# Performance work log

Measured on AMD Instinct MI355X. Metric: run time of the kernel, lower is better.

## Reference

```python
import jax, jax.numpy as jnp
import numpy as np

B, S, E = 2, 2048, 1024
HID = 1024
HEADS = 16
EPS = 1e-5
SCALE = (E * 2) ** (-0.5)  # source uses input_data_dim*2


def setup_inputs() -> dict:
    key = jax.random.key(0)
    k1, k2, k3 = jax.random.split(key, 3)
    return {
        "x": jax.random.normal(k1, (B, S, E), dtype=jnp.float32),
        "ln_g": jnp.ones((E,), jnp.float32),
        "ln_b": jnp.zeros((E,), jnp.float32),
        "W1": jax.random.normal(k2, (E, 3 * HID), jnp.float32) * 0.02,
        "b1": jnp.zeros((3 * HID,), jnp.float32),
        "W2": jax.random.normal(k3, (HID, HID), jnp.float32) * 0.02,
        "b2": jnp.zeros((HID,), jnp.float32),
    }


def reference(x, ln_g, ln_b, W1, b1, W2, b2):
    # LayerNorm over last dim
    mu = jnp.mean(x, axis=-1, keepdims=True)
    var = jnp.mean(jnp.square(x - mu), axis=-1, keepdims=True)
    xn = (x - mu) * jax.lax.rsqrt(var + EPS) * ln_g + ln_b
    # QKV projection: [B,S,3*HID]
    qkv = jnp.einsum('bse,ef->bsf', xn, W1) + b1
    # Faithful to source: flat reshape to (heads, B, S, 3*HID/heads)
    qkv_heads = qkv.reshape(HEADS, B, S, -1)
    q, k, v = jnp.split(qkv_heads, 3, axis=-1)  # each [H,B,S,d]
    scores = jnp.einsum('hbse,hbSe->hbsS', q, k) * SCALE  # [H,B,S,S]
    att = jax.nn.softmax(scores, axis=-1)
    full_att = jnp.einsum('hbsS,hbSe->hbse', att, v)  # [H,B,S,d]
    full_att = full_att.reshape(B, S, -1)  # faithful flat reshape -> [B,S,HID]
    out = jnp.einsum('bsh,hk->bsk', full_att, W2) + b2
    return out
```

## Files before the change

kernel.cpp:

```cpp
#include <hip/hip_runtime.h>

typedef unsigned short u16;
typedef __bf16 bf16x8 __attribute__((ext_vector_type(8)));
typedef float f32x4 __attribute__((ext_vector_type(4)));

static constexpr float SCALE2 = 0.022097086912079608f * 1.4426950408889634f;

__device__ __forceinline__ u16 f2b(float f) {
  union { float f; unsigned int i; } v; v.f = f;
  unsigned int r = v.i + 0x7fffu + ((v.i >> 16) & 1u);
  return (u16)(r >> 16);
}
__device__ __forceinline__ unsigned int pk2(float a, float b) {
#if __has_builtin(__builtin_amdgcn_cvt_pk_bf16_f32)
  auto v = __builtin_amdgcn_cvt_pk_bf16_f32(a, b);
  unsigned int u;
  __builtin_memcpy(&u, &v, 4);
  return u;
#else
  union { float f; unsigned int i; } x, y; x.f = a; y.f = b;
  return ((x.i + 0x8000u) >> 16) | ((y.i + 0x8000u) & 0xffff0000u);
#endif
}
__device__ __forceinline__ void async16(const u16* g, u16* l) {
  __builtin_amdgcn_global_load_lds((const __attribute__((address_space(1))) void*)g,
                                   (__attribute__((address_space(3))) void*)l,
                                   16, 0, 0);
}

__global__ __launch_bounds__(256) void ln_kernel(const float* __restrict__ x,
                                                 const float* __restrict__ g,
                                                 const float* __restrict__ b,
                                                 u16* __restrict__ xn) {
  const int row = blockIdx.x;
  const int t = threadIdx.x;
  float4 v = *(const float4*)(x + (size_t)row * 1024 + t * 4);
  float s = v.x + v.y + v.z + v.w;
  float ss = v.x * v.x + v.y * v.y + v.z * v.z + v.w * v.w;
  for (int off = 32; off >= 1; off >>= 1) {
    s += __shfl_xor(s, off, 64);
    ss += __shfl_xor(ss, off, 64);
  }
  __shared__ float red[8];
  const int w = t >> 6;
  if ((t & 63) == 0) { red[w] = s; red[4 + w] = ss; }
  __syncthreads();
  s = red[0] + red[1] + red[2] + red[3];
  ss = red[4] + red[5] + red[6] + red[7];
  const float mu = s * (1.0f / 1024.0f);
  const float var = ss * (1.0f / 1024.0f) - mu * mu;
  const float inv = rsqrtf(var + 1e-5f);
  float4 gg = *(const float4*)(g + t * 4);
  float4 bb = *(const float4*)(b + t * 4);
  ushort4 o;
  o.x = f2b((v.x - mu) * inv * gg.x + bb.x);
  o.y = f2b((v.y - mu) * inv * gg.y + bb.y);
  o.z = f2b((v.z - mu) * inv * gg.z + bb.z);
  o.w = f2b((v.w - mu) * inv * gg.w + bb.w);
  *(ushort4*)(xn + (size_t)row * 1024 + t * 4) = o;
}

__global__ __launch_bounds__(256) void transpose2_k(const float* __restrict__ W1,
                                                    u16* __restrict__ W1T,
                                                    const float* __restrict__ W2,
                                                    u16* __restrict__ W2T) {
  const int z = blockIdx.z;
  if (z == 1 && blockIdx.x >= 16) return;
  const int C = z ? 1024 : 3072;
  const float* in = z ? W2 : W1;
  u16* out = z ? W2T : W1T;
  __shared__ u16 tile[64 * 72];
  const int c0 = blockIdx.x * 64, r0 = blockIdx.y * 64;
  const int t = threadIdx.x;
  const int row = t >> 2, cseg = t & 3;
  for (int it = 0; it < 4; it++) {
    float4 v = *(const float4*)&in[(size_t)(r0 + row) * C + c0 + it * 16 + cseg * 4];
    ushort4 o;
    o.x = f2b(v.x); o.y = f2b(v.y); o.z = f2b(v.z); o.w = f2b(v.w);
    *(ushort4*)&tile[row * 72 + it * 16 + cseg * 4] = o;
  }
  __syncthreads();
  const int orow = t >> 2, ch = t & 3;
  u16 vals[16];
  for (int j = 0; j < 16; j++) vals[j] = tile[(ch * 16 + j) * 72 + orow];
  u16* dp = out + (size_t)(c0 + orow) * 1024 + r0 + ch * 16;
  *(uint4*)&dp[0] = *(uint4*)&vals[0];
  *(uint4*)&dp[8] = *(uint4*)&vals[8];
}

template <int MODE, int MT>
__global__ __launch_bounds__(256) void gemm_bt(const u16* __restrict__ A,
                                               const u16* __restrict__ Bt,
                                               const float* __restrict__ bias,
                                               float* __restrict__ C,
                                               int M, int N, int K,
                                               u16* __restrict__ Qc,
                                               u16* __restrict__ Kc,
                                               u16* __restrict__ Vtmp) {
  __shared__ __align__(16) u16 SMEM[8192];
  u16* As = SMEM;
  u16* Bs = SMEM + MT * 32;
  const int m0 = blockIdx.y * MT, n0 = blockIdx.x * 128;
  const int t = threadIdx.x, w = t >> 6, lane = t & 63;
  const int q = lane >> 4, l16 = lane & 15;
  const int wm = (w >> 1) * (MT / 2), wn = (w & 1) * 64;
  constexpr int NI = MT / 32;

  const int sc = (lane & 3) ^ ((lane >> 3) & 3);
  const u16* ap = A + (size_t)(m0 + w * 16 + (lane >> 2)) * K + sc * 8;
  const u16* bp = Bt + (size_t)(n0 + w * 16 + (lane >> 2)) * K + sc * 8;
  u16* lA = &As[w * 512];
  u16* lB = &Bs[w * 512];
  const int ac = q ^ ((l16 >> 1) & 3);

  f32x4 acc[NI][4];
  const f32x4 zero = {0.f, 0.f, 0.f, 0.f};
  for (int i = 0; i < NI; i++)
    for (int j = 0; j < 4; j++) acc[i][j] = zero;

  for (int k0 = 0; k0 < K; k0 += 32) {
    for (int i = 0; i < MT / 64; i++)
      async16(ap + (size_t)(i * 64) * K, lA + i * 2048);
    for (int i = 0; i < 2; i++)
      async16(bp + (size_t)(i * 64) * K, lB + i * 2048);
    ap += 32; bp += 32;
    __syncthreads();
    bf16x8 af[NI], bfr[4];
    for (int i = 0; i < NI; i++)
      af[i] = *(const bf16x8*)&As[(wm + i * 16 + l16) * 32 + ac * 8];
    for (int j = 0; j < 4; j++)
      bfr[j] = *(const bf16x8*)&Bs[(wn + j * 16 + l16) * 32 + ac * 8];
    for (int i = 0; i < NI; i++)
      for (int j = 0; j < 4; j++)
        acc[i][j] = __builtin_amdgcn_mfma_f32_16x16x32_bf16(af[i], bfr[j], acc[i][j], 0, 0, 0);
    __syncthreads();
  }

  if constexpr (MODE == 0) {
    for (int j = 0; j < 4; j++) {
      const int col = n0 + wn + j * 16 + l16;
      const float bv = bias[col];
      for (int i = 0; i < NI; i++) {
        const int rbase = m0 + wm + i * 16 + q * 4;
        for (int r = 0; r < 4; r++)
          C[(size_t)(rbase + r) * N + col] = acc[i][j][r] + bv;
      }
    }
  } else {
    const int seg = n0 + wn;
    const int k64 = seg >> 6;
    const int tcol = k64 / 3;
    const int typ = k64 - tcol * 3;
    u16* dst = (typ == 0) ? Qc : (typ == 1) ? Kc : Vtmp;
    const int gidx = m0 >> 7;
    u16* tw = &SMEM[w * 1280];
    float bv[4];
    for (int j = 0; j < 4; j++) bv[j] = bias[seg + j * 16 + l16];
    __syncthreads();
    for (int i = 0; i < 4; i++) {
      for (int j = 0; j < 4; j++) {
        ushort4 pk;
        pk.x = f2b(acc[i][j][0] + bv[j]);
        pk.y = f2b(acc[i][j][1] + bv[j]);
        pk.z = f2b(acc[i][j][2] + bv[j]);
        pk.w = f2b(acc[i][j][3] + bv[j]);
        *(ushort4*)&tw[(j * 16 + l16) * 20 + q * 4] = pk;
      }
      const int r2 = lane >> 2;
      const int quarter = lane & 3;
      u16 vals[16];
      for (int c = 0; c < 16; c++)
        vals[c] = tw[(quarter * 16 + c) * 20 + r2];
      const int lr = wm + i * 16 + r2;
      const int s = (lr << 4) + tcol;
      u16* dp = dst + ((size_t)gidx * 2048 + s) * 64 + quarter * 16;
      *(uint4*)&dp[0] = *(uint4*)&vals[0];
      *(uint4*)&dp[8] = *(uint4*)&vals[8];
    }
  }
}

__global__ __launch_bounds__(256) void vtrans(const u16* __restrict__ Vtmp,
                                              u16* __restrict__ Vt) {
  __shared__ __align__(16) u16 tile[64 * 64];
  const int g = blockIdx.y, s0 = blockIdx.x * 64;
  const int t = threadIdx.x;
  const int row = t >> 3, ch = t & 7;
  for (int p = 0; p < 2; p++) {
    const int r = p * 32 + row;
    uint4 v = *(const uint4*)&Vtmp[((size_t)g * 2048 + s0 + r) * 64 + ch * 8];
    *(uint4*)&tile[r * 64 + ((ch ^ (r & 7)) * 8)] = v;
  }
  __syncthreads();
  const int d = t >> 2, scn = t & 3;
  u16 vals[16];
  for (int j2 = 0; j2 < 16; j2++) {
    const int s = scn * 16 + j2;
    vals[j2] = tile[s * 64 + (((d >> 3) ^ (s & 7)) * 8) + (d & 7)];
  }
  u16* dp = Vt + ((size_t)g * 64 + d) * 2048 + s0 + scn * 16;
  *(uint4*)&dp[0] = *(uint4*)&vals[0];
  *(uint4*)&dp[8] = *(uint4*)&vals[8];
}

__global__ __launch_bounds__(256) void attn_kernel(const u16* __restrict__ Qc,
                                                   const u16* __restrict__ Kc,
                                                   const u16* __restrict__ Vt,
                                                   u16* __restrict__ Oc) {
  __shared__ __align__(16) u16 LDS[32768];
  u16* Ks = LDS;
  u16* Vs = LDS + 8192;
  u16* Ps = LDS + 16384;
  const int g = blockIdx.y;
  const int q0 = blockIdx.x * 128;
  const int t = threadIdx.x, w = t >> 6, lane = t & 63;
  const int q = lane >> 4, l16 = lane & 15;

  const u16* Qg = Qc + (size_t)g * 2048 * 64;
  const u16* Kg = Kc + (size_t)g * 2048 * 64;
  const u16* Vg = Vt + (size_t)g * 64 * 2048;

  bf16x8 aq[2][2];
  for (int rt = 0; rt < 2; rt++)
    for (int ks = 0; ks < 2; ks++)
      aq[rt][ks] = *(const bf16x8*)&Qg[(size_t)(q0 + w * 32 + rt * 16 + l16) * 64 + ks * 32 + q * 8];

  f32x4 accO[2][4];
  const f32x4 zero = {0.f, 0.f, 0.f, 0.f};
  for (int rt = 0; rt < 2; rt++)
    for (int c = 0; c < 4; c++) accO[rt][c] = zero;
  f32x4 psv[2] = {zero, zero};

  const int kc = (lane & 7) ^ ((lane >> 3) & 7);
  const int vc = (lane & 15) ^ ((w * 4 + (lane >> 4)) & 7);
  const u16* kp = Kg + (size_t)(w * 8 + (lane >> 3)) * 64 + kc * 8;
  const u16* vp = Vg + (size_t)(w * 4 + (lane >> 4)) * 2048 + vc * 8;
  u16* lK = &Ks[w * 512];
  u16* lV = &Vs[w * 512];

  const int kch = q ^ (l16 & 7);
  const int pbase = w * 4096;
  const int pxor = l16 & 3;

  for (int it = 0; it < 16; it++) {
    const int kt0 = it * 128;
    for (int i = 0; i < 4; i++) {
      async16(kp + (size_t)kt0 * 64 + i * 2048, lK + i * 2048);
      async16(vp + kt0 + (size_t)i * 32768, lV + i * 2048);
    }
    __syncthreads();

    f32x4 sa[2][8];
    for (int ct = 0; ct < 8; ct++) {
      bf16x8 bk0 = *(const bf16x8*)&Ks[(ct * 16 + l16) * 64 + kch * 8];
      bf16x8 bk1 = *(const bf16x8*)&Ks[(ct * 16 + l16) * 64 + (kch ^ 4) * 8];
      for (int rt = 0; rt < 2; rt++) {
        f32x4 a = zero;
        a = __builtin_amdgcn_mfma_f32_16x16x32_bf16(bk0, aq[rt][0], a, 0, 0, 0);
        a = __builtin_amdgcn_mfma_f32_16x16x32_bf16(bk1, aq[rt][1], a, 0, 0, 0);
        sa[rt][ct] = a;
      }
    }

    for (int rt = 0; rt < 2; rt++) {
      const int sbase = pbase + rt * 2048 + l16 * 32;
      for (int ct = 0; ct < 8; ct++) {
        f32x4 p;
        for (int r = 0; r < 4; r++) p[r] = __builtin_amdgcn_exp2f(sa[rt][ct][r] * SCALE2);
        psv[rt] += p;
        uint2 pk;
        pk.x = pk2(p[0], p[1]);
        pk.y = pk2(p[2], p[3]);
        const int c2 = ((ct & 1) * 2 + (q >> 1)) ^ pxor;
        *(uint2*)&Ps[sbase + (ct >> 1) * 512 + c2 * 8 + (q & 1) * 4] = pk;
      }
    }

    for (int ks2 = 0; ks2 < 4; ks2++) {
      bf16x8 apf[2];
      for (int rt = 0; rt < 2; rt++)
        apf[rt] = *(const bf16x8*)&Ps[pbase + rt * 2048 + ks2 * 512 + l16 * 32 + (q ^ pxor) * 8];
      for (int c = 0; c < 4; c++) {
        const int vch = (ks2 * 4 + q) ^ (l16 & 7);
        bf16x8 bv = *(const bf16x8*)&Vs[(c * 16 + l16) * 128 + vch * 8];
        for (int rt = 0; rt < 2; rt++)
          accO[rt][c] = __builtin_amdgcn_mfma_f32_16x16x32_bf16(bv, apf[rt], accO[rt][c], 0, 0, 0);
      }
    }
    __syncthreads();
  }

  for (int rt = 0; rt < 2; rt++) {
    float lsum = psv[rt][0] + psv[rt][1] + psv[rt][2] + psv[rt][3];
    lsum += __shfl_xor(lsum, 16, 64);
    lsum += __shfl_xor(lsum, 32, 64);
    const int srow = q0 + w * 32 + rt * 16 + l16;
    const int orow = g * 128 + (srow >> 4);
    const int cbase = (srow & 15) * 64;
    const float linv = 1.0f / lsum;
    for (int c = 0; c < 4; c++) {
      ushort4 o;
      o.x = f2b(accO[rt][c][0] * linv);
      o.y = f2b(accO[rt][c][1] * linv);
      o.z = f2b(accO[rt][c][2] * linv);
      o.w = f2b(accO[rt][c][3] * linv);
      *(ushort4*)&Oc[(size_t)orow * 1024 + cbase + c * 16 + q * 4] = o;
    }
  }
}

extern "C" void kernel_launch(void* const* d_in, const int* in_sizes, int n_in,
                              void* d_out, int out_size, void* d_ws, size_t ws_size,
                              hipStream_t stream) {
  (void)in_sizes; (void)n_in; (void)out_size; (void)ws_size;
  const float* x    = (const float*)d_in[0];
  const float* ln_g = (const float*)d_in[1];
  const float* ln_b = (const float*)d_in[2];
  const float* W1   = (const float*)d_in[3];
  const float* b1   = (const float*)d_in[4];
  const float* W2   = (const float*)d_in[5];
  const float* b2   = (const float*)d_in[6];

  char* ws = (char*)d_ws;
  u16* xn   = (u16*)(ws);
  u16* W1T  = (u16*)(ws + ((size_t)8 << 20));
  u16* W2T  = (u16*)(ws + ((size_t)14 << 20));
  u16* Qc   = (u16*)(ws + ((size_t)16 << 20));
  u16* Kc   = (u16*)(ws + ((size_t)24 << 20));
  u16* Vtmp = (u16*)(ws + ((size_t)32 << 20));
  u16* Vt   = (u16*)(ws + ((size_t)40 << 20));
  u16* Oc   = xn;

  ln_kernel<<<dim3(4096), dim3(256), 0, stream>>>(x, ln_g, ln_b, xn);
  transpose2_k<<<dim3(48, 16, 2), dim3(256), 0, stream>>>(W1, W1T, W2, W2T);
  gemm_bt<1, 128><<<dim3(24, 32), dim3(256), 0, stream>>>(xn, W1T, b1, nullptr,
                                                          4096, 3072, 1024, Qc, Kc, Vtmp);
  vtrans<<<dim3(32, 32), dim3(256), 0, stream>>>(Vtmp, Vt);
  attn_kernel<<<dim3(16, 32), dim3(256), 0, stream>>>(Qc, Kc, Vt, Oc);
  gemm_bt<0, 64><<<dim3(8, 64), dim3(256), 0, stream>>>(Oc, W2T, b2, (float*)d_out,
                                                        4096, 1024, 1024, nullptr, nullptr, nullptr);
}
```

Measured before the change: 209.6 us.

## Split attention over two key halves with a combine pass, fold scale into Q

The attention kernel now processes each query block against only half of the keys (grid z = 2), writing unnormalized bf16 partial outputs and row sums, and a new combine kernel adds the two halves and normalizes. The P buffer in LDS is halved by computing softmax probabilities and the PV product in two phases, which allows more resident blocks. The softmax scale is folded into Q in the QKV GEMM epilogue, removing a multiply per score. This doubles the attention grid to improve occupancy and parallelism, at the cost of an extra kernel launch, extra global traffic for the partials, and bf16 rounding of the unnormalized partials. It relies on the existing code taking no max subtraction in the softmax.

```diff
diff --git a/kernel.cpp b/kernel.cpp
--- a/kernel.cpp
+++ b/kernel.cpp
@@ -10,6 +10,9 @@
   union { float f; unsigned int i; } v; v.f = f;
   unsigned int r = v.i + 0x7fffu + ((v.i >> 16) & 1u);
   return (u16)(r >> 16);
+}
+__device__ __forceinline__ float b2f(u16 u) {
+  union { unsigned int i; float f; } v; v.i = ((unsigned int)u) << 16; return v.f;
 }
 __device__ __forceinline__ unsigned int pk2(float a, float b) {
 #if __has_builtin(__builtin_amdgcn_cvt_pk_bf16_f32)
@@ -152,6 +155,7 @@
     const int tcol = k64 / 3;
     const int typ = k64 - tcol * 3;
     u16* dst = (typ == 0) ? Qc : (typ == 1) ? Kc : Vtmp;
+    const float qs = (typ == 0) ? SCALE2 : 1.0f;
     const int gidx = m0 >> 7;
     u16* tw = &SMEM[w * 1280];
     float bv[4];
@@ -160,10 +164,10 @@
     for (int i = 0; i < 4; i++) {
       for (int j = 0; j < 4; j++) {
         ushort4 pk;
-        pk.x = f2b(acc[i][j][0] + bv[j]);
-        pk.y = f2b(acc[i][j][1] + bv[j]);
-        pk.z = f2b(acc[i][j][2] + bv[j]);
-        pk.w = f2b(acc[i][j][3] + bv[j]);
+        pk.x = f2b((acc[i][j][0] + bv[j]) * qs);
+        pk.y = f2b((acc[i][j][1] + bv[j]) * qs);
+        pk.z = f2b((acc[i][j][2] + bv[j]) * qs);
+        pk.w = f2b((acc[i][j][3] + bv[j]) * qs);
         *(ushort4*)&tw[(j * 16 + l16) * 20 + q * 4] = pk;
       }
       const int r2 = lane >> 2;
@@ -206,19 +210,22 @@
 __global__ __launch_bounds__(256) void attn_kernel(const u16* __restrict__ Qc,
                                                    const u16* __restrict__ Kc,
                                                    const u16* __restrict__ Vt,
-                                                   u16* __restrict__ Oc) {
-  __shared__ __align__(16) u16 LDS[32768];
+                                                   u16* __restrict__ Op,
+                                                   float* __restrict__ lp)
+{
+  __shared__ __align__(16) u16 LDS[24576];
   u16* Ks = LDS;
   u16* Vs = LDS + 8192;
   u16* Ps = LDS + 16384;
   const int g = blockIdx.y;
   const int q0 = blockIdx.x * 128;
+  const int half = blockIdx.z;
   const int t = threadIdx.x, w = t >> 6, lane = t & 63;
   const int q = lane >> 4, l16 = lane & 15;
 
   const u16* Qg = Qc + (size_t)g * 2048 * 64;
-  const u16* Kg = Kc + (size_t)g * 2048 * 64;
-  const u16* Vg = Vt + (size_t)g * 64 * 2048;
+  const u16* Kg = Kc + (size_t)g * 2048 * 64 + (size_t)half * 1024 * 64;
+  const u16* Vg = Vt + (size_t)g * 64 * 2048 + half * 1024;
 
   bf16x8 aq[2][2];
   for (int rt = 0; rt < 2; rt++)
@@ -239,10 +246,10 @@
   u16* lV = &Vs[w * 512];
 
   const int kch = q ^ (l16 & 7);
-  const int pbase = w * 4096;
+  const int pbase = w * 2048;
   const int pxor = l16 & 3;
 
-  for (int it = 0; it < 16; it++) {
+  for (int it = 0; it < 8; it++) {
     const int kt0 = it * 128;
     for (int i = 0; i < 4; i++) {
       async16(kp + (size_t)kt0 * 64 + i * 2048, lK + i * 2048);
@@ -262,51 +269,73 @@
       }
     }
 
-    for (int rt = 0; rt < 2; rt++) {
-      const int sbase = pbase + rt * 2048 + l16 * 32;
-      for (int ct = 0; ct < 8; ct++) {
-        f32x4 p;
-        for (int r = 0; r < 4; r++) p[r] = __builtin_amdgcn_exp2f(sa[rt][ct][r] * SCALE2);
-        psv[rt] += p;
-        uint2 pk;
-        pk.x = pk2(p[0], p[1]);
-        pk.y = pk2(p[2], p[3]);
-        const int c2 = ((ct & 1) * 2 + (q >> 1)) ^ pxor;
-        *(uint2*)&Ps[sbase + (ct >> 1) * 512 + c2 * 8 + (q & 1) * 4] = pk;
-      }
-    }
-
-    for (int ks2 = 0; ks2 < 4; ks2++) {
-      bf16x8 apf[2];
-      for (int rt = 0; rt < 2; rt++)
-        apf[rt] = *(const bf16x8*)&Ps[pbase + rt * 2048 + ks2 * 512 + l16 * 32 + (q ^ pxor) * 8];
-      for (int c = 0; c < 4; c++) {
-        const int vch = (ks2 * 4 + q) ^ (l16 & 7);
-        bf16x8 bv = *(const bf16x8*)&Vs[(c * 16 + l16) * 128 + vch * 8];
+    for (int ph = 0; ph < 2; ph++) {
+      for (int rt = 0; rt < 2; rt++) {
+        const int sbase = pbase + rt * 1024 + l16 * 32;
+        for (int c4 = 0; c4 < 4; c4++) {
+          const int ct = ph * 4 + c4;
+          f32x4 p;
+          for (int r = 0; r < 4; r++) p[r] = __builtin_amdgcn_exp2f(sa[rt][ct][r]);
+          psv[rt] += p;
+          uint2 pk;
+          pk.x = pk2(p[0], p[1]);
+          pk.y = pk2(p[2], p[3]);
+          const int c2 = ((c4 & 1) * 2 + (q >> 1)) ^ pxor;
+          *(uint2*)&Ps[sbase + (c4 >> 1) * 512 + c2 * 8 + (q & 1) * 4] = pk;
+        }
+      }
+      for (int k2 = 0; k2 < 2; k2++) {
+        const int ks2 = ph * 2 + k2;
+        bf16x8 apf[2];
         for (int rt = 0; rt < 2; rt++)
-          accO[rt][c] = __builtin_amdgcn_mfma_f32_16x16x32_bf16(bv, apf[rt], accO[rt][c], 0, 0, 0);
-      }
-    }
-    __syncthreads();
-  }
-
+          apf[rt] = *(const bf16x8*)&Ps[pbase + rt * 1024 + k2 * 512 + l16 * 32 + (q ^ pxor) * 8];
+        for (int c = 0; c < 4; c++) {
+          const int vch = (ks2 * 4 + q) ^ (l16 & 7);
+          bf16x8 bv = *(const bf16x8*)&Vs[(c * 16 + l16) * 128 + vch * 8];
+          for (int rt = 0; rt < 2; rt++)
+            accO[rt][c] = __builtin_amdgcn_mfma_f32_16x16x32_bf16(bv, apf[rt], accO[rt][c], 0, 0, 0);
+        }
+      }
+    }
+    __syncthreads();
+  }
+
+  u16* Oh = Op + (size_t)half * 4194304;
   for (int rt = 0; rt < 2; rt++) {
     float lsum = psv[rt][0] + psv[rt][1] + psv[rt][2] + psv[rt][3];
     lsum += __shfl_xor(lsum, 16, 64);
     lsum += __shfl_xor(lsum, 32, 64);
     const int srow = q0 + w * 32 + rt * 16 + l16;
+    if (q == 0) lp[half * 65536 + g * 2048 + srow] = lsum;
     const int orow = g * 128 + (srow >> 4);
     const int cbase = (srow & 15) * 64;
-    const float linv = 1.0f / lsum;
     for (int c = 0; c < 4; c++) {
       ushort4 o;
-      o.x = f2b(accO[rt][c][0] * linv);
-      o.y = f2b(accO[rt][c][1] * linv);
-      o.z = f2b(accO[rt][c][2] * linv);
-      o.w = f2b(accO[rt][c][3] * linv);
-      *(ushort4*)&Oc[(size_t)orow * 1024 + cbase + c * 16 + q * 4] = o;
-    }
-  }
+      o.x = f2b(accO[rt][c][0]);
+      o.y = f2b(accO[rt][c][1]);
+      o.z = f2b(accO[rt][c][2]);
+      o.w = f2b(accO[rt][c][3]);
+      *(ushort4*)&Oh[(size_t)orow * 1024 + cbase + c * 16 + q * 4] = o;
+    }
+  }
+}
+
+__global__ __launch_bounds__(256) void combine_k(const u16* __restrict__ Op,
+                                                 const float* __restrict__ lp,
+                                                 u16* __restrict__ Oc) {
+  const int idx4 = (blockIdx.x * 256 + threadIdx.x) * 4;
+  const int orow = idx4 >> 10, col = idx4 & 1023;
+  const int g = orow >> 7, shi = orow & 127, slo = col >> 6;
+  const int s = g * 2048 + shi * 16 + slo;
+  const float inv = 1.0f / (lp[s] + lp[65536 + s]);
+  ushort4 a = *(const ushort4*)&Op[(size_t)idx4];
+  ushort4 b = *(const ushort4*)&Op[(size_t)4194304 + idx4];
+  ushort4 o;
+  o.x = f2b((b2f(a.x) + b2f(b.x)) * inv);
+  o.y = f2b((b2f(a.y) + b2f(b.y)) * inv);
+  o.z = f2b((b2f(a.z) + b2f(b.z)) * inv);
+  o.w = f2b((b2f(a.w) + b2f(b.w)) * inv);
+  *(ushort4*)&Oc[(size_t)idx4] = o;
 }
 
 extern "C" void kernel_launch(void* const* d_in, const int* in_sizes, int n_in,
@@ -329,6 +358,8 @@
   u16* Kc   = (u16*)(ws + ((size_t)24 << 20));
   u16* Vtmp = (u16*)(ws + ((size_t)32 << 20));
   u16* Vt   = (u16*)(ws + ((size_t)40 << 20));
+  u16* Op   = Vtmp;
+  float* lp = (float*)(ws + ((size_t)56 << 20));
   u16* Oc   = xn;
 
   ln_kernel<<<dim3(4096), dim3(256), 0, stream>>>(x, ln_g, ln_b, xn);
@@ -336,7 +367,8 @@
   gemm_bt<1, 128><<<dim3(24, 32), dim3(256), 0, stream>>>(xn, W1T, b1, nullptr,
                                                           4096, 3072, 1024, Qc, Kc, Vtmp);
   vtrans<<<dim3(32, 32), dim3(256), 0, stream>>>(Vtmp, Vt);
-  attn_kernel<<<dim3(16, 32), dim3(256), 0, stream>>>(Qc, Kc, Vt, Oc);
+  attn_kernel<<<dim3(16, 32, 2), dim3(256), 0, stream>>>(Qc, Kc, Vt, Op, lp);
+  combine_k<<<dim3(4096), dim3(256), 0, stream>>>(Op, lp, Oc);
   gemm_bt<0, 64><<<dim3(8, 64), dim3(256), 0, stream>>>(Oc, W2T, b2, (float*)d_out,
                                                         4096, 1024, 1024, nullptr, nullptr, nullptr);
 }
```

Result: slower. 214.6 us (+2.4%).

## Merge LN and weight transpose kernels, fold softmax scale into Q, shrink P buffer

Applied to the files above, without the earlier changes.

Combines the LayerNorm and weight-transpose launches into one kernel with a flat grid, removing a launch. Pre-multiplies Q by the softmax scale (times log2 e) in the QKV GEMM epilogue, so attention no longer multiplies each score before exp2. The attention P staging buffer is halved by processing P in two phases of 64 columns with padded rows instead of XOR swizzle, reducing LDS per block (which may allow more blocks per CU). Rounding Q to bf16 after scaling slightly changes numerics.

```diff
diff --git a/kernel.cpp b/kernel.cpp
--- a/kernel.cpp
+++ b/kernel.cpp
@@ -28,61 +28,68 @@
                                    16, 0, 0);
 }
 
-__global__ __launch_bounds__(256) void ln_kernel(const float* __restrict__ x,
-                                                 const float* __restrict__ g,
-                                                 const float* __restrict__ b,
-                                                 u16* __restrict__ xn) {
-  const int row = blockIdx.x;
+__global__ __launch_bounds__(256) void pre_kernel(const float* __restrict__ x,
+                                                  const float* __restrict__ lg,
+                                                  const float* __restrict__ lb,
+                                                  u16* __restrict__ xn,
+                                                  const float* __restrict__ W1,
+                                                  u16* __restrict__ W1T,
+                                                  const float* __restrict__ W2,
+                                                  u16* __restrict__ W2T) {
+  __shared__ __align__(16) u16 smem[64 * 72];
+  const int bx = blockIdx.x;
   const int t = threadIdx.x;
-  float4 v = *(const float4*)(x + (size_t)row * 1024 + t * 4);
-  float s = v.x + v.y + v.z + v.w;
-  float ss = v.x * v.x + v.y * v.y + v.z * v.z + v.w * v.w;
-  for (int off = 32; off >= 1; off >>= 1) {
-    s += __shfl_xor(s, off, 64);
-    ss += __shfl_xor(ss, off, 64);
-  }
-  __shared__ float red[8];
-  const int w = t >> 6;
-  if ((t & 63) == 0) { red[w] = s; red[4 + w] = ss; }
-  __syncthreads();
-  s = red[0] + red[1] + red[2] + red[3];
-  ss = red[4] + red[5] + red[6] + red[7];
-  const float mu = s * (1.0f / 1024.0f);
-  const float var = ss * (1.0f / 1024.0f) - mu * mu;
-  const float inv = rsqrtf(var + 1e-5f);
-  float4 gg = *(const float4*)(g + t * 4);
-  float4 bb = *(const float4*)(b + t * 4);
-  ushort4 o;
-  o.x = f2b((v.x - mu) * inv * gg.x + bb.x);
-  o.y = f2b((v.y - mu) * inv * gg.y + bb.y);
-  o.z = f2b((v.z - mu) * inv * gg.z + bb.z);
-  o.w = f2b((v.w - mu) * inv * gg.w + bb.w);
-  *(ushort4*)(xn + (size_t)row * 1024 + t * 4) = o;
-}
-
-__global__ __launch_bounds__(256) void transpose2_k(const float* __restrict__ W1,
-                                                    u16* __restrict__ W1T,
-                                                    const float* __restrict__ W2,
-                                                    u16* __restrict__ W2T) {
-  const int z = blockIdx.z;
-  if (z == 1 && blockIdx.x >= 16) return;
-  const int C = z ? 1024 : 3072;
-  const float* in = z ? W2 : W1;
-  u16* out = z ? W2T : W1T;
-  __shared__ u16 tile[64 * 72];
-  const int c0 = blockIdx.x * 64, r0 = blockIdx.y * 64;
-  const int t = threadIdx.x;
+  if (bx < 4096) {
+    float* red = (float*)smem;
+    const int row = bx;
+    float4 v = *(const float4*)(x + (size_t)row * 1024 + t * 4);
+    float s = v.x + v.y + v.z + v.w;
+    float ss = v.x * v.x + v.y * v.y + v.z * v.z + v.w * v.w;
+    for (int off = 32; off >= 1; off >>= 1) {
+      s += __shfl_xor(s, off, 64);
+      ss += __shfl_xor(ss, off, 64);
+    }
+    const int w = t >> 6;
+    if ((t & 63) == 0) { red[w] = s; red[4 + w] = ss; }
+    __syncthreads();
+    s = red[0] + red[1] + red[2] + red[3];
+    ss = red[4] + red[5] + red[6] + red[7];
+    const float mu = s * (1.0f / 1024.0f);
+    const float var = ss * (1.0f / 1024.0f) - mu * mu;
+    const float inv = rsqrtf(var + 1e-5f);
+    float4 gg = *(const float4*)(lg + t * 4);
+    float4 bb = *(const float4*)(lb + t * 4);
+    ushort4 o;
+    o.x = f2b((v.x - mu) * inv * gg.x + bb.x);
+    o.y = f2b((v.y - mu) * inv * gg.y + bb.y);
+    o.z = f2b((v.z - mu) * inv * gg.z + bb.z);
+    o.w = f2b((v.w - mu) * inv * gg.w + bb.w);
+    *(ushort4*)(xn + (size_t)row * 1024 + t * 4) = o;
+    return;
+  }
+  const float* in;
+  u16* out;
+  int C, c0, r0;
+  if (bx < 4096 + 768) {
+    const int idx = bx - 4096;
+    C = 3072; in = W1; out = W1T;
+    c0 = (idx % 48) * 64; r0 = (idx / 48) * 64;
+  } else {
+    const int idx = bx - 4864;
+    C = 1024; in = W2; out = W2T;
+    c0 = (idx % 16) * 64; r0 = (idx / 16) * 64;
+  }
   const int row = t >> 2, cseg = t & 3;
   for (int it = 0; it < 4; it++) {
     float4 v = *(const float4*)&in[(size_t)(r0 + row) * C + c0 + it * 16 + cseg * 4];
     ushort4 o;
     o.x = f2b(v.x); o.y = f2b(v.y); o.z = f2b(v.z); o.w = f2b(v.w);
-    *(ushort4*)&tile[row * 72 + it * 16 + cseg * 4] = o;
+    *(ushort4*)&smem[row * 72 + it * 16 + cseg * 4] = o;
   }
   __syncthreads();
   const int orow = t >> 2, ch = t & 3;
   u16 vals[16];
-  for (int j = 0; j < 16; j++) vals[j] = tile[(ch * 16 + j) * 72 + orow];
+  for (int j = 0; j < 16; j++) vals[j] = smem[(ch * 16 + j) * 72 + orow];
   u16* dp = out + (size_t)(c0 + orow) * 1024 + r0 + ch * 16;
   *(uint4*)&dp[0] = *(uint4*)&vals[0];
   *(uint4*)&dp[8] = *(uint4*)&vals[8];
@@ -152,6 +159,7 @@
     const int tcol = k64 / 3;
     const int typ = k64 - tcol * 3;
     u16* dst = (typ == 0) ? Qc : (typ == 1) ? Kc : Vtmp;
+    const float qs = (typ == 0) ? SCALE2 : 1.0f;
     const int gidx = m0 >> 7;
     u16* tw = &SMEM[w * 1280];
     float bv[4];
@@ -160,10 +168,10 @@
     for (int i = 0; i < 4; i++) {
       for (int j = 0; j < 4; j++) {
         ushort4 pk;
-        pk.x = f2b(acc[i][j][0] + bv[j]);
-        pk.y = f2b(acc[i][j][1] + bv[j]);
-        pk.z = f2b(acc[i][j][2] + bv[j]);
-        pk.w = f2b(acc[i][j][3] + bv[j]);
+        pk.x = f2b((acc[i][j][0] + bv[j]) * qs);
+        pk.y = f2b((acc[i][j][1] + bv[j]) * qs);
+        pk.z = f2b((acc[i][j][2] + bv[j]) * qs);
+        pk.w = f2b((acc[i][j][3] + bv[j]) * qs);
         *(ushort4*)&tw[(j * 16 + l16) * 20 + q * 4] = pk;
       }
       const int r2 = lane >> 2;
@@ -207,7 +215,7 @@
                                                    const u16* __restrict__ Kc,
                                                    const u16* __restrict__ Vt,
                                                    u16* __restrict__ Oc) {
-  __shared__ __align__(16) u16 LDS[32768];
+  __shared__ __align__(16) u16 LDS[25600];
   u16* Ks = LDS;
   u16* Vs = LDS + 8192;
   u16* Ps = LDS + 16384;
@@ -239,8 +247,7 @@
   u16* lV = &Vs[w * 512];
 
   const int kch = q ^ (l16 & 7);
-  const int pbase = w * 4096;
-  const int pxor = l16 & 3;
+  const int pb = w * 2304;
 
   for (int it = 0; it < 16; it++) {
     const int kt0 = it * 128;
@@ -262,29 +269,31 @@
       }
     }
 
-    for (int rt = 0; rt < 2; rt++) {
-      const int sbase = pbase + rt * 2048 + l16 * 32;
-      for (int ct = 0; ct < 8; ct++) {
-        f32x4 p;
-        for (int r = 0; r < 4; r++) p[r] = __builtin_amdgcn_exp2f(sa[rt][ct][r] * SCALE2);
-        psv[rt] += p;
-        uint2 pk;
-        pk.x = pk2(p[0], p[1]);
-        pk.y = pk2(p[2], p[3]);
-        const int c2 = ((ct & 1) * 2 + (q >> 1)) ^ pxor;
-        *(uint2*)&Ps[sbase + (ct >> 1) * 512 + c2 * 8 + (q & 1) * 4] = pk;
-      }
-    }
-
-    for (int ks2 = 0; ks2 < 4; ks2++) {
-      bf16x8 apf[2];
-      for (int rt = 0; rt < 2; rt++)
-        apf[rt] = *(const bf16x8*)&Ps[pbase + rt * 2048 + ks2 * 512 + l16 * 32 + (q ^ pxor) * 8];
-      for (int c = 0; c < 4; c++) {
-        const int vch = (ks2 * 4 + q) ^ (l16 & 7);
-        bf16x8 bv = *(const bf16x8*)&Vs[(c * 16 + l16) * 128 + vch * 8];
+    for (int ph = 0; ph < 2; ph++) {
+      for (int rt = 0; rt < 2; rt++) {
+        u16* Pr = &Ps[pb + rt * 1152 + l16 * 72];
+        for (int c4 = 0; c4 < 4; c4++) {
+          const int ct = ph * 4 + c4;
+          f32x4 p;
+          for (int r = 0; r < 4; r++) p[r] = __builtin_amdgcn_exp2f(sa[rt][ct][r]);
+          psv[rt] += p;
+          uint2 pk;
+          pk.x = pk2(p[0], p[1]);
+          pk.y = pk2(p[2], p[3]);
+          *(uint2*)&Pr[c4 * 16 + q * 4] = pk;
+        }
+      }
+      for (int k2 = 0; k2 < 2; k2++) {
+        const int ks2 = ph * 2 + k2;
+        bf16x8 apf[2];
         for (int rt = 0; rt < 2; rt++)
-          accO[rt][c] = __builtin_amdgcn_mfma_f32_16x16x32_bf16(bv, apf[rt], accO[rt][c], 0, 0, 0);
+          apf[rt] = *(const bf16x8*)&Ps[pb + rt * 1152 + l16 * 72 + k2 * 32 + q * 8];
+        for (int c = 0; c < 4; c++) {
+          const int vch = (ks2 * 4 + q) ^ (l16 & 7);
+          bf16x8 bv = *(const bf16x8*)&Vs[(c * 16 + l16) * 128 + vch * 8];
+          for (int rt = 0; rt < 2; rt++)
+            accO[rt][c] = __builtin_amdgcn_mfma_f32_16x16x32_bf16(bv, apf[rt], accO[rt][c], 0, 0, 0);
+        }
       }
     }
     __syncthreads();
@@ -331,8 +340,7 @@
   u16* Vt   = (u16*)(ws + ((size_t)40 << 20));
   u16* Oc   = xn;
 
-  ln_kernel<<<dim3(4096), dim3(256), 0, stream>>>(x, ln_g, ln_b, xn);
-  transpose2_k<<<dim3(48, 16, 2), dim3(256), 0, stream>>>(W1, W1T, W2, W2T);
+  pre_kernel<<<dim3(5120), dim3(256), 0, stream>>>(x, ln_g, ln_b, xn, W1, W1T, W2, W2T);
   gemm_bt<1, 128><<<dim3(24, 32), dim3(256), 0, stream>>>(xn, W1T, b1, nullptr,
                                                           4096, 3072, 1024, Qc, Kc, Vtmp);
   vtrans<<<dim3(32, 32), dim3(256), 0, stream>>>(Vtmp, Vt);
```

Result: no change. 208.7 us (-0.5%).
